# Kernel optimization log

Hardware: AMD Instinct MI355X
Metric: run time of the kernel (lower is better)

Reference implementation:

```python
import jax, jax.numpy as jnp
import numpy as np

EMBED_DIM = 1024
NUM_HEADS = 16
HEAD_DIM = EMBED_DIM // NUM_HEADS


def setup_inputs() -> dict:
    key = jax.random.key(0)
    ks = jax.random.split(key, 12)
    B, S, D = 4, 2048, EMBED_DIM
    scale = 1.0 / np.sqrt(D)
    inp = {
        "query": jax.random.normal(ks[0], (B, S, D), jnp.float32),
        "key": jax.random.normal(ks[1], (B, S, D), jnp.float32),
        "value": jax.random.normal(ks[2], (B, S, D), jnp.float32),
        # nn.Linear weights: [out_features, in_features], y = x @ W.T + b
        "Wq": jax.random.normal(ks[3], (D, D), jnp.float32) * scale,
        "bq": jnp.zeros((D,), jnp.float32),
        "Wk": jax.random.normal(ks[4], (D, D), jnp.float32) * scale,
        "bk": jnp.zeros((D,), jnp.float32),
        "Wv": jax.random.normal(ks[5], (D, D), jnp.float32) * scale,
        "bv": jnp.zeros((D,), jnp.float32),
        "Wo": jax.random.normal(ks[6], (D, D), jnp.float32) * scale,
        "bo": jnp.zeros((D,), jnp.float32),
    }
    return inp


def reference(query, key, value, Wq, bq, Wk, bk, Wv, bv, Wo, bo):
    B, Sq, D = query.shape
    Sk = key.shape[1]
    H, Dh = NUM_HEADS, HEAD_DIM

    def proj(x, W, b):
        # [B,S,D] -> [B,H,S,Dh]
        y = jnp.einsum('bsd,ed->bse', x, W) + b
        return y.reshape(x.shape[0], x.shape[1], H, Dh).transpose(0, 2, 1, 3)

    q = proj(query, Wq, bq)
    k = proj(key, Wk, bk)
    v = proj(value, Wv, bv)

    # sigmoid attention (no softmax); dropout is identity in eval mode
    scores = jnp.einsum('bhqd,bhkd->bhqk', q, k) / jnp.sqrt(jnp.float32(Dh)).astype(q.dtype)
    attn = jax.nn.sigmoid(scores)
    out = jnp.einsum('bhqk,bhkd->bhqd', attn, v)

    out = out.transpose(0, 2, 1, 3).reshape(B, Sq, D)
    return jnp.einsum('bsd,ed->bse', out, Wo) + bo
```

## Files before the change

### kernel.cpp

```cpp
#include <hip/hip_runtime.h>


typedef _Float16 f16x2 __attribute__((ext_vector_type(2)));
typedef _Float16 f16x4 __attribute__((ext_vector_type(4)));
typedef _Float16 f16x8 __attribute__((ext_vector_type(8)));
typedef __fp16   h16x2 __attribute__((ext_vector_type(2)));
typedef float    f32x4 __attribute__((ext_vector_type(4)));
typedef float    f32x16 __attribute__((ext_vector_type(16)));

typedef __attribute__((address_space(3))) void* lds_vp;
typedef const __attribute__((address_space(1))) void* gbl_vp;

__device__ __forceinline__ void gld_lds16(const void* g, void* l) {
  __builtin_amdgcn_global_load_lds((gbl_vp)g, (lds_vp)l, 16, 0, 0);
}

__device__ __forceinline__ f16x8 cvt8(float4 a, float4 b) {
  return (f16x8){(_Float16)a.x, (_Float16)a.y, (_Float16)a.z, (_Float16)a.w,
                 (_Float16)b.x, (_Float16)b.y, (_Float16)b.z, (_Float16)b.w};
}

__device__ __forceinline__ f16x2 pk2(float a, float b) {
  h16x2 r = __builtin_amdgcn_cvt_pkrtz(a, b);
  return __builtin_bit_cast(f16x2, r);
}

__device__ __forceinline__ float exp2_fast(float x) {
#if __has_builtin(__builtin_amdgcn_exp2f)
  return __builtin_amdgcn_exp2f(x);
#else
  float r;
  asm("v_exp_f32 %0, %1" : "=v"(r) : "v"(x));
  return r;
#endif
}

#define BM 128
#define BN 128
#define BK 32

template <bool AF16, bool BF16, bool TRANSV, bool OUTF32>
__global__ __launch_bounds__(256) void gemm_bt(const void* __restrict__ Av,
                                               const void* __restrict__ Bv,
                                               const float* __restrict__ bias,
                                               void* __restrict__ Yv,
                                               int M, int N, int K) {
  __shared__ __align__(16) _Float16 sA[BM * BK];
  __shared__ __align__(16) _Float16 sB[BN * BK];

  const int t = threadIdx.x, lane = t & 63, wid = t >> 6;
  const int m0 = blockIdx.x * BM, n0 = blockIdx.y * BN;
  const int wm = (wid >> 1) * 64, wn = (wid & 1) * 64;
  const int lrow = lane & 15, g = lane >> 4;

  f32x4 acc[4][4] = {};

  const int arow = 16 * wid + (lane >> 2);
  const int gq = (lane & 3) ^ ((lane >> 3) & 3);
  _Float16* lA1 = sA + wid * 512;
  _Float16* lA2 = sA + 2048 + wid * 512;
  _Float16* lB1 = sB + wid * 512;
  _Float16* lB2 = sB + 2048 + wid * 512;

  const int mrow = t >> 1, mhalf = t & 1;
  const int mm = (mrow >> 1) & 3;
  const int ch_lo = mrow * 4 + ((2 * mhalf) ^ mm);
  const int ch_hi = ch_lo ^ 1;

  const _Float16* pA16a = nullptr; const _Float16* pA16b = nullptr;
  const float* pA32 = nullptr;
  if constexpr (AF16) {
    const _Float16* A = (const _Float16*)Av;
    pA16a = A + (size_t)(m0 + arow) * K + gq * 8;
    pA16b = A + (size_t)(m0 + 64 + arow) * K + gq * 8;
  } else {
    pA32 = (const float*)Av + (size_t)(m0 + mrow) * K + mhalf * 16;
  }
  const _Float16* pB16a = nullptr; const _Float16* pB16b = nullptr;
  const float* pB32 = nullptr;
  if constexpr (BF16) {
    const _Float16* B = (const _Float16*)Bv;
    pB16a = B + (size_t)(n0 + arow) * K + gq * 8;
    pB16b = B + (size_t)(n0 + 64 + arow) * K + gq * 8;
  } else {
    pB32 = (const float*)Bv + (size_t)(n0 + mrow) * K + mhalf * 16;
  }

  const int xr = g ^ ((lrow >> 1) & 3);

  for (int k0 = 0; k0 < K; k0 += BK) {
    float4 av[4], bv4[4];
    if constexpr (!AF16) {
      const float4* p = (const float4*)(pA32 + k0);
      av[0] = p[0]; av[1] = p[1]; av[2] = p[2]; av[3] = p[3];
    }
    if constexpr (!BF16) {
      const float4* p = (const float4*)(pB32 + k0);
      bv4[0] = p[0]; bv4[1] = p[1]; bv4[2] = p[2]; bv4[3] = p[3];
    }
    __syncthreads();
    if constexpr (AF16) {
      gld_lds16(pA16a + k0, lA1);
      gld_lds16(pA16b + k0, lA2);
    } else {
      *(f16x8*)(sA + ch_lo * 8) = cvt8(av[0], av[1]);
      *(f16x8*)(sA + ch_hi * 8) = cvt8(av[2], av[3]);
    }
    if constexpr (BF16) {
      gld_lds16(pB16a + k0, lB1);
      gld_lds16(pB16b + k0, lB2);
    } else {
      *(f16x8*)(sB + ch_lo * 8) = cvt8(bv4[0], bv4[1]);
      *(f16x8*)(sB + ch_hi * 8) = cvt8(bv4[2], bv4[3]);
    }
    __syncthreads();

    f16x8 af[4], bf[4];
#pragma unroll
    for (int i = 0; i < 4; i++)
      af[i] = *(const f16x8*)(sA + (wm + i * 16 + lrow) * 32 + xr * 8);
#pragma unroll
    for (int j = 0; j < 4; j++)
      bf[j] = *(const f16x8*)(sB + (wn + j * 16 + lrow) * 32 + xr * 8);
#pragma unroll
    for (int i = 0; i < 4; i++)
#pragma unroll
      for (int j = 0; j < 4; j++)
        acc[i][j] = __builtin_amdgcn_mfma_f32_16x16x32_f16(af[i], bf[j], acc[i][j], 0, 0, 0);
  }

  const int orow = g * 4, ocol = lrow;
#pragma unroll
  for (int j = 0; j < 4; j++) {
    const int col = n0 + wn + j * 16 + ocol;
    const float bv = bias[col];
#pragma unroll
    for (int i = 0; i < 4; i++) {
      const int row = m0 + wm + i * 16 + orow;
      if constexpr (TRANSV) {
        _Float16* VT = (_Float16*)Yv;
        int s = row & 2047;
        int sp = (s & ~12) | ((s & 4) << 1) | ((s & 8) >> 1);
        _Float16* dst = VT + (((size_t)(row >> 11) * 16 + (col >> 6)) * 64 + (col & 63)) * 2048 + sp;
        f16x4 v = {(_Float16)(acc[i][j][0] + bv), (_Float16)(acc[i][j][1] + bv),
                   (_Float16)(acc[i][j][2] + bv), (_Float16)(acc[i][j][3] + bv)};
        *(f16x4*)dst = v;
      } else if constexpr (OUTF32) {
        float* Y = (float*)Yv;
#pragma unroll
        for (int r = 0; r < 4; r++) Y[(size_t)(row + r) * N + col] = acc[i][j][r] + bv;
      } else {
        _Float16* Y = (_Float16*)Yv;
#pragma unroll
        for (int r = 0; r < 4; r++) Y[(size_t)(row + r) * N + col] = (_Float16)(acc[i][j][r] + bv);
      }
    }
  }
}

__global__ __launch_bounds__(256) void qkv_gemm(const _Float16* __restrict__ Xq,
                                                const _Float16* __restrict__ Xk,
                                                const _Float16* __restrict__ Xv,
                                                const _Float16* __restrict__ W,
                                                const float* __restrict__ bq,
                                                const float* __restrict__ bk,
                                                const float* __restrict__ bv,
                                                _Float16* __restrict__ Qo,
                                                _Float16* __restrict__ Ko,
                                                _Float16* __restrict__ VT) {
  __shared__ __align__(16) _Float16 sA[BM * BK];
  __shared__ __align__(16) _Float16 sB[BN * BK];

  const int t = threadIdx.x, lane = t & 63, wid = t >> 6;
  const int n0g = blockIdx.x * BN, m0 = blockIdx.y * BM;
  const int seg = blockIdx.x >> 3, n0 = n0g & 1023;
  const _Float16* A = (seg == 0) ? Xq : (seg == 1) ? Xk : Xv;
  const float* bias = (seg == 0) ? bq : (seg == 1) ? bk : bv;
  const int K = 1024;

  const int wm = (wid >> 1) * 64, wn = (wid & 1) * 64;
  const int lrow = lane & 15, g = lane >> 4;

  f32x4 acc[4][4] = {};

  const int arow = 16 * wid + (lane >> 2);
  const int gq = (lane & 3) ^ ((lane >> 3) & 3);
  _Float16* lA1 = sA + wid * 512;
  _Float16* lA2 = sA + 2048 + wid * 512;
  _Float16* lB1 = sB + wid * 512;
  _Float16* lB2 = sB + 2048 + wid * 512;

  const _Float16* pA16a = A + (size_t)(m0 + arow) * K + gq * 8;
  const _Float16* pA16b = A + (size_t)(m0 + 64 + arow) * K + gq * 8;
  const _Float16* pB16a = W + (size_t)(n0g + arow) * K + gq * 8;
  const _Float16* pB16b = W + (size_t)(n0g + 64 + arow) * K + gq * 8;

  const int xr = g ^ ((lrow >> 1) & 3);

  for (int k0 = 0; k0 < K; k0 += BK) {
    __syncthreads();
    gld_lds16(pA16a + k0, lA1);
    gld_lds16(pA16b + k0, lA2);
    gld_lds16(pB16a + k0, lB1);
    gld_lds16(pB16b + k0, lB2);
    __syncthreads();

    f16x8 af[4], bf[4];
#pragma unroll
    for (int i = 0; i < 4; i++)
      af[i] = *(const f16x8*)(sA + (wm + i * 16 + lrow) * 32 + xr * 8);
#pragma unroll
    for (int j = 0; j < 4; j++)
      bf[j] = *(const f16x8*)(sB + (wn + j * 16 + lrow) * 32 + xr * 8);
#pragma unroll
    for (int i = 0; i < 4; i++)
#pragma unroll
      for (int j = 0; j < 4; j++)
        acc[i][j] = __builtin_amdgcn_mfma_f32_16x16x32_f16(af[i], bf[j], acc[i][j], 0, 0, 0);
  }

  const int orow = g * 4, ocol = lrow;
#pragma unroll
  for (int j = 0; j < 4; j++) {
    const int col = n0 + wn + j * 16 + ocol;
    const float bvv = bias[col];
#pragma unroll
    for (int i = 0; i < 4; i++) {
      const int row = m0 + wm + i * 16 + orow;
      if (seg == 2) {
        int s = row & 2047;
        int sp = (s & ~12) | ((s & 4) << 1) | ((s & 8) >> 1);
        _Float16* dst = VT + (((size_t)(row >> 11) * 16 + (col >> 6)) * 64 + (col & 63)) * 2048 + sp;
        f16x4 v = {(_Float16)(acc[i][j][0] + bvv), (_Float16)(acc[i][j][1] + bvv),
                   (_Float16)(acc[i][j][2] + bvv), (_Float16)(acc[i][j][3] + bvv)};
        *(f16x4*)dst = v;
      } else {
        _Float16* Y = (seg == 0) ? Qo : Ko;
#pragma unroll
        for (int r = 0; r < 4; r++) Y[(size_t)(row + r) * 1024 + col] = (_Float16)(acc[i][j][r] + bvv);
      }
    }
  }
}

#define LDS_ROW 72

template <int KSPL>
__global__ __launch_bounds__(256, 4) void attn_sig(const _Float16* __restrict__ Q,
                                                   const _Float16* __restrict__ K,
                                                   const _Float16* __restrict__ VT,
                                                   _Float16* __restrict__ O) {
  __shared__ __align__(16) _Float16 smem[128 * LDS_ROW];
  _Float16* sK = smem;
  _Float16* sVT = smem + 64 * LDS_ROW;

  constexpr int SKEY = 2048 / KSPL;

  const int t = threadIdx.x, lane = t & 63, wid = t >> 6;
  const int l31 = lane & 31, g5 = lane >> 5;
  const int b = blockIdx.z, h = blockIdx.y;
  const int qb = (KSPL == 2) ? (int)(blockIdx.x >> 1) : (int)blockIdx.x;
  const int kh = (KSPL == 2) ? (int)(blockIdx.x & 1) : 0;
  const int q0 = qb * 128;
  const int qw = q0 + wid * 32;

  f16x8 qf[4];
  {
    const _Float16* qp = Q + (size_t)(b * 2048 + qw + l31) * 1024 + h * 64;
#pragma unroll
    for (int dhc = 0; dhc < 4; dhc++)
      qf[dhc] = *(const f16x8*)(qp + dhc * 16 + g5 * 8) * (_Float16)-0.18033688f;
  }

  f32x16 oacc[2] = {};

  const int srow = t >> 2, scol = (t & 3) * 16;
  const _Float16* kbase = K + ((size_t)(b * 2048) + kh * SKEY + srow) * 1024 + h * 64 + scol;
  const _Float16* vbase = VT + ((size_t)((b * 16 + h) * 64 + srow)) * 2048 + kh * SKEY + scol;

  uint4 ka = *(const uint4*)kbase;
  uint4 kb = *(const uint4*)(kbase + 8);
  uint4 va = *(const uint4*)vbase;
  uint4 vb = *(const uint4*)(vbase + 8);

  for (int kt = 0; kt < SKEY; kt += 64) {
    __syncthreads();
    *(uint4*)&sK[srow * LDS_ROW + scol] = ka;
    *(uint4*)&sK[srow * LDS_ROW + scol + 8] = kb;
    *(uint4*)&sVT[srow * LDS_ROW + scol] = va;
    *(uint4*)&sVT[srow * LDS_ROW + scol + 8] = vb;
    __syncthreads();

    const int kt2 = kt + 64;
    if (kt2 < SKEY) {
      ka = *(const uint4*)(kbase + (size_t)kt2 * 1024);
      kb = *(const uint4*)(kbase + (size_t)kt2 * 1024 + 8);
      va = *(const uint4*)(vbase + kt2);
      vb = *(const uint4*)(vbase + kt2 + 8);
    }

#pragma unroll
    for (int kt32 = 0; kt32 < 2; kt32++) {
      f16x8 kf[4];
#pragma unroll
      for (int dhc = 0; dhc < 4; dhc++)
        kf[dhc] = *(const f16x8*)&sK[(kt32 * 32 + l31) * LDS_ROW + dhc * 16 + g5 * 8];

      f32x16 sacc = {};
      __builtin_amdgcn_s_setprio(1);
#pragma unroll
      for (int dhc = 0; dhc < 4; dhc++)
        sacc = __builtin_amdgcn_mfma_f32_32x32x16_f16(kf[dhc], qf[dhc], sacc, 0, 0, 0);
      __builtin_amdgcn_s_setprio(0);

      f16x8 pf[2];
#pragma unroll
      for (int G = 0; G < 2; G++) {
        union { f16x8 v; f16x2 h[4]; } u;
#pragma unroll
        for (int pr = 0; pr < 4; pr++) {
          float e0 = exp2_fast(sacc[G * 8 + pr * 2 + 0]);
          float e1 = exp2_fast(sacc[G * 8 + pr * 2 + 1]);
          u.h[pr] = pk2(__builtin_amdgcn_rcpf(1.0f + e0),
                        __builtin_amdgcn_rcpf(1.0f + e1));
        }
        pf[G] = u.v;
      }

      __builtin_amdgcn_s_setprio(1);
#pragma unroll
      for (int dht = 0; dht < 2; dht++)
#pragma unroll
        for (int G = 0; G < 2; G++) {
          f16x8 vf = *(const f16x8*)&sVT[(dht * 32 + l31) * LDS_ROW + kt32 * 32 + G * 16 + g5 * 8];
          oacc[dht] = __builtin_amdgcn_mfma_f32_32x32x16_f16(vf, pf[G], oacc[dht], 0, 0, 0);
        }
      __builtin_amdgcn_s_setprio(0);
    }
  }

  _Float16* Ob = O + (size_t)kh * (8192 * 1024);
  __syncthreads();
  _Float16* ep = smem;
#pragma unroll
  for (int dht = 0; dht < 2; dht++)
#pragma unroll
    for (int c = 0; c < 4; c++) {
      f16x4 o4 = {(_Float16)oacc[dht][4 * c + 0], (_Float16)oacc[dht][4 * c + 1],
                  (_Float16)oacc[dht][4 * c + 2], (_Float16)oacc[dht][4 * c + 3]};
      *(f16x4*)&ep[(wid * 32 + l31) * LDS_ROW + dht * 32 + c * 8 + g5 * 4] = o4;
    }
  __syncthreads();
#pragma unroll
  for (int i = 0; i < 4; i++) {
    const int q = i * 32 + (t >> 3), dhc = t & 7;
    f16x8 row = *(const f16x8*)&ep[q * LDS_ROW + dhc * 8];
    *(f16x8*)(Ob + (size_t)(b * 2048 + q0 + q) * 1024 + h * 64 + dhc * 8) = row;
  }
}

__global__ __launch_bounds__(256) void add_halves(const _Float16* __restrict__ a,
                                                  const _Float16* __restrict__ b,
                                                  _Float16* __restrict__ o, int n) {
  const int i = (blockIdx.x * 256 + threadIdx.x) * 8;
  if (i >= n) return;
  f16x8 x = *(const f16x8*)(a + i);
  f16x8 y = *(const f16x8*)(b + i);
  *(f16x8*)(o + i) = x + y;
}

struct CvtArgs {
  const float* src[7];
  _Float16* dst[7];
  int n[7];
  int cnt;
};

__global__ __launch_bounds__(256) void cvt_f32_f16(CvtArgs a) {
  const int ti = blockIdx.y;
  if (ti >= a.cnt) return;
  const int i = (blockIdx.x * 256 + threadIdx.x) * 8;
  if (i >= a.n[ti]) return;
  const float4* s = (const float4*)(a.src[ti] + i);
  float4 x = s[0], y = s[1];
  *(f16x8*)(a.dst[ti] + i) = cvt8(x, y);
}

extern "C" void kernel_launch(void* const* d_in, const int* in_sizes, int n_in,
                              void* d_out, int out_size, void* d_ws, size_t ws_size,
                              hipStream_t stream) {
  const float* query = (const float*)d_in[0];
  const float* key   = (const float*)d_in[1];
  const float* value = (const float*)d_in[2];
  const float* Wq = (const float*)d_in[3];
  const float* bq = (const float*)d_in[4];
  const float* Wk = (const float*)d_in[5];
  const float* bk = (const float*)d_in[6];
  const float* Wv = (const float*)d_in[7];
  const float* bv = (const float*)d_in[8];
  const float* Wo = (const float*)d_in[9];
  const float* bo = (const float*)d_in[10];
  float* out = (float*)d_out;

  const int D = 1024, M = 8192;
  const size_t MB = 1024 * 1024;
  char* ws = (char*)d_ws;
  dim3 bb(256);

  if (ws_size >= 104 * MB) {
    _Float16* Xq = (_Float16*)(ws + 0 * MB);
    _Float16* Xk = (_Float16*)(ws + 16 * MB);
    _Float16* Xv = (_Float16*)(ws + 32 * MB);
    _Float16* Qp = (_Float16*)(ws + 48 * MB);
    _Float16* Kp = (_Float16*)(ws + 64 * MB);
    _Float16* VT = (_Float16*)(ws + 80 * MB);
    _Float16* Wf = (_Float16*)(ws + 96 * MB);
    _Float16* AO0 = Xq;
    _Float16* AO1 = Xk;
    _Float16* AO  = Xv;
    CvtArgs ca{};
    ca.src[0] = query; ca.dst[0] = Xq; ca.n[0] = M * D;
    ca.src[1] = key;   ca.dst[1] = Xk; ca.n[1] = M * D;
    ca.src[2] = value; ca.dst[2] = Xv; ca.n[2] = M * D;
    ca.src[3] = Wq; ca.dst[3] = Wf + 0 * 1048576; ca.n[3] = D * D;
    ca.src[4] = Wk; ca.dst[4] = Wf + 1 * 1048576; ca.n[4] = D * D;
    ca.src[5] = Wv; ca.dst[5] = Wf + 2 * 1048576; ca.n[5] = D * D;
    ca.src[6] = Wo; ca.dst[6] = Wf + 3 * 1048576; ca.n[6] = D * D;
    ca.cnt = 7;
    cvt_f32_f16<<<dim3(4096, 7), bb, 0, stream>>>(ca);
    qkv_gemm<<<dim3(24, 64), bb, 0, stream>>>(Xq, Xk, Xv, Wf, bq, bk, bv, Qp, Kp, VT);
    attn_sig<2><<<dim3(32, 16, 4), bb, 0, stream>>>(Qp, Kp, VT, AO0);
    add_halves<<<dim3(4096), bb, 0, stream>>>(AO0, AO1, AO, M * D);
    gemm_bt<true, true, false, true><<<dim3(64, 8), bb, 0, stream>>>(AO, Wf + 3 * 1048576, bo, out, M, D, D);
  } else {
    _Float16* Qp = (_Float16*)(ws + 0 * MB);
    _Float16* Kp = (_Float16*)(ws + 16 * MB);
    _Float16* VT = (_Float16*)(ws + 32 * MB);
    _Float16* AO = (_Float16*)(ws + 48 * MB);
    gemm_bt<false, false, false, false><<<dim3(64, 8), bb, 0, stream>>>(query, Wq, bq, Qp, M, D, D);
    gemm_bt<false, false, false, false><<<dim3(64, 8), bb, 0, stream>>>(key,   Wk, bk, Kp, M, D, D);
    gemm_bt<false, false, true,  false><<<dim3(64, 8), bb, 0, stream>>>(value, Wv, bv, VT, M, D, D);
    attn_sig<1><<<dim3(16, 16, 4), bb, 0, stream>>>(Qp, Kp, VT, AO);
    gemm_bt<true, false, false, true><<<dim3(64, 8), bb, 0, stream>>>(AO, Wo, bo, out, M, D, D);
  }
}
```

Measured before the change: 369.2 us.

## Load V fragments directly from global memory instead of staging through LDS

The attention kernel stops staging V^T tiles in shared memory. Each wave now reads its V fragments straight from global memory (VT is already transposed, so the fragment layout matches), and the output epilogue is split into two halves so it fits in the smaller LDS buffer. This halves LDS use per block, which could allow more resident blocks, and removes the V LDS writes and reads. In exchange every wave issues redundant global and L2 loads of V, and those loads are not prefetched a tile ahead, so memory latency may sit on the MFMA critical path.

Measured after the change: 403.2 us. +9.2%, slower.

```diff
diff --git a/kernel.cpp b/kernel.cpp
--- a/kernel.cpp
+++ b/kernel.cpp
@@ -250,9 +250,8 @@
                                                    const _Float16* __restrict__ K,
                                                    const _Float16* __restrict__ VT,
                                                    _Float16* __restrict__ O) {
-  __shared__ __align__(16) _Float16 smem[128 * LDS_ROW];
+  __shared__ __align__(16) _Float16 smem[64 * LDS_ROW];
   _Float16* sK = smem;
-  _Float16* sVT = smem + 64 * LDS_ROW;
 
   constexpr int SKEY = 2048 / KSPL;
 
@@ -276,31 +275,33 @@
 
   const int srow = t >> 2, scol = (t & 3) * 16;
   const _Float16* kbase = K + ((size_t)(b * 2048) + kh * SKEY + srow) * 1024 + h * 64 + scol;
-  const _Float16* vbase = VT + ((size_t)((b * 16 + h) * 64 + srow)) * 2048 + kh * SKEY + scol;
+  const _Float16* Vg = VT + (size_t)((b * 16 + h) * 64) * 2048 + kh * SKEY;
+  const _Float16* Vrow = Vg + (size_t)l31 * 2048 + g5 * 8;
 
   uint4 ka = *(const uint4*)kbase;
   uint4 kb = *(const uint4*)(kbase + 8);
-  uint4 va = *(const uint4*)vbase;
-  uint4 vb = *(const uint4*)(vbase + 8);
 
   for (int kt = 0; kt < SKEY; kt += 64) {
     __syncthreads();
     *(uint4*)&sK[srow * LDS_ROW + scol] = ka;
     *(uint4*)&sK[srow * LDS_ROW + scol + 8] = kb;
-    *(uint4*)&sVT[srow * LDS_ROW + scol] = va;
-    *(uint4*)&sVT[srow * LDS_ROW + scol + 8] = vb;
     __syncthreads();
 
     const int kt2 = kt + 64;
     if (kt2 < SKEY) {
       ka = *(const uint4*)(kbase + (size_t)kt2 * 1024);
       kb = *(const uint4*)(kbase + (size_t)kt2 * 1024 + 8);
-      va = *(const uint4*)(vbase + kt2);
-      vb = *(const uint4*)(vbase + kt2 + 8);
     }
 
 #pragma unroll
     for (int kt32 = 0; kt32 < 2; kt32++) {
+      f16x8 vf[2][2];
+#pragma unroll
+      for (int dht = 0; dht < 2; dht++)
+#pragma unroll
+        for (int G = 0; G < 2; G++)
+          vf[dht][G] = *(const f16x8*)(Vrow + (size_t)dht * 65536 + kt + kt32 * 32 + G * 16);
+
       f16x8 kf[4];
 #pragma unroll
       for (int dhc = 0; dhc < 4; dhc++)
@@ -331,31 +332,35 @@
 #pragma unroll
       for (int dht = 0; dht < 2; dht++)
 #pragma unroll
-        for (int G = 0; G < 2; G++) {
-          f16x8 vf = *(const f16x8*)&sVT[(dht * 32 + l31) * LDS_ROW + kt32 * 32 + G * 16 + g5 * 8];
-          oacc[dht] = __builtin_amdgcn_mfma_f32_32x32x16_f16(vf, pf[G], oacc[dht], 0, 0, 0);
+        for (int G = 0; G < 2; G++)
+          oacc[dht] = __builtin_amdgcn_mfma_f32_32x32x16_f16(vf[dht][G], pf[G], oacc[dht], 0, 0, 0);
+      __builtin_amdgcn_s_setprio(0);
+    }
+  }
+
+  _Float16* Ob = O + (size_t)kh * (8192 * 1024);
+#pragma unroll
+  for (int half = 0; half < 2; half++) {
+    __syncthreads();
+    if ((wid >> 1) == half) {
+      const int qr = (wid & 1) * 32 + l31;
+#pragma unroll
+      for (int dht = 0; dht < 2; dht++)
+#pragma unroll
+        for (int c = 0; c < 4; c++) {
+          f16x4 o4 = {(_Float16)oacc[dht][4 * c + 0], (_Float16)oacc[dht][4 * c + 1],
+                      (_Float16)oacc[dht][4 * c + 2], (_Float16)oacc[dht][4 * c + 3]};
+          *(f16x4*)&smem[qr * LDS_ROW + dht * 32 + c * 8 + g5 * 4] = o4;
         }
-      __builtin_amdgcn_s_setprio(0);
-    }
-  }
-
-  _Float16* Ob = O + (size_t)kh * (8192 * 1024);
-  __syncthreads();
-  _Float16* ep = smem;
-#pragma unroll
-  for (int dht = 0; dht < 2; dht++)
-#pragma unroll
-    for (int c = 0; c < 4; c++) {
-      f16x4 o4 = {(_Float16)oacc[dht][4 * c + 0], (_Float16)oacc[dht][4 * c + 1],
-                  (_Float16)oacc[dht][4 * c + 2], (_Float16)oacc[dht][4 * c + 3]};
-      *(f16x4*)&ep[(wid * 32 + l31) * LDS_ROW + dht * 32 + c * 8 + g5 * 4] = o4;
-    }
-  __syncthreads();
-#pragma unroll
-  for (int i = 0; i < 4; i++) {
-    const int q = i * 32 + (t >> 3), dhc = t & 7;
-    f16x8 row = *(const f16x8*)&ep[q * LDS_ROW + dhc * 8];
-    *(f16x8*)(Ob + (size_t)(b * 2048 + q0 + q) * 1024 + h * 64 + dhc * 8) = row;
+    }
+    __syncthreads();
+#pragma unroll
+    for (int i = 0; i < 2; i++) {
+      const int qr = i * 32 + (t >> 3), dhc = t & 7;
+      const int q = half * 64 + qr;
+      f16x8 row = *(const f16x8*)&smem[qr * LDS_ROW + dhc * 8];
+      *(f16x8*)(Ob + (size_t)(b * 2048 + q0 + q) * 1024 + h * 64 + dhc * 8) = row;
+    }
   }
 }
 
```
